# Performance work log

Measured on AMD Instinct MI355X. Metric: run time of the kernel, lower is better.

## Reference

```python
import jax, jax.numpy as jnp
import numpy as np

FACTOR = 0.5  # matches init_kwargs factor


def setup_inputs() -> dict:
    key = jax.random.key(0)
    k1, k2 = jax.random.split(key)
    E, D, N = 1600000, 32, 100000
    edge_data = jax.random.normal(k1, (E, D), dtype=jnp.float32)
    edge_dst = jax.random.randint(k2, (E,), 0, N, dtype=jnp.int64)
    return {"edge_data": edge_data, "edge_dst": edge_dst, "num_nodes": N}


def reference(edge_data, edge_dst, num_nodes):
    # EdgewiseReduce.forward: optional scalar premultiply, then scatter-sum
    # edge features into per-node bins by destination index.
    scaled = edge_data * FACTOR                     # [E, D]
    out = jax.ops.segment_sum(scaled, edge_dst, num_segments=num_nodes)  # [N, D]
    return out
```

## Files before the change

### kernel.cpp

```cpp
#include <hip/hip_runtime.h>
#include <hip/hip_bf16.h>


#define D 32
#define FACTOR 0.5f
#define BSHIFT 7
#define BNODES (1 << BSHIFT)
#define CAPSHIFT 12
#define CAP (1 << CAPSHIFT)

#define S_THREADS 512
#define S_PER_T 2
__global__ __launch_bounds__(S_THREADS)
void scatter_kernel(const int* __restrict__ dst, int* __restrict__ gcursor,
                    int* __restrict__ order, int2* __restrict__ ovf,
                    int* __restrict__ ovf_count, int E, int N, int nb) {
  extern __shared__ int sm[];
  int* lhist = sm;
  int* lcur = sm + nb;
  const int4* dst4 = (const int4*)dst;
  const int n4 = E >> 2;
  const int base4 = blockIdx.x * (S_THREADS * S_PER_T);
  const int i4a = base4 + threadIdx.x;
  const int i4b = i4a + S_THREADS;
  const bool tail_block = (blockIdx.x == gridDim.x - 1);

  for (int i = threadIdx.x; i < nb; i += S_THREADS) lhist[i] = 0;
  __syncthreads();

  int4 va, vb;
  bool ha = (i4a < n4), hb = (i4b < n4);
  if (ha) {
    va = dst4[i4a];
    if ((unsigned)va.x < (unsigned)N) atomicAdd(&lhist[va.x >> BSHIFT], 1);
    if ((unsigned)va.y < (unsigned)N) atomicAdd(&lhist[va.y >> BSHIFT], 1);
    if ((unsigned)va.z < (unsigned)N) atomicAdd(&lhist[va.z >> BSHIFT], 1);
    if ((unsigned)va.w < (unsigned)N) atomicAdd(&lhist[va.w >> BSHIFT], 1);
  }
  if (hb) {
    vb = dst4[i4b];
    if ((unsigned)vb.x < (unsigned)N) atomicAdd(&lhist[vb.x >> BSHIFT], 1);
    if ((unsigned)vb.y < (unsigned)N) atomicAdd(&lhist[vb.y >> BSHIFT], 1);
    if ((unsigned)vb.z < (unsigned)N) atomicAdd(&lhist[vb.z >> BSHIFT], 1);
    if ((unsigned)vb.w < (unsigned)N) atomicAdd(&lhist[vb.w >> BSHIFT], 1);
  }
  if (tail_block) {
    for (int e = (n4 << 2) + threadIdx.x; e < E; e += S_THREADS) {
      int d = dst[e];
      if ((unsigned)d < (unsigned)N) atomicAdd(&lhist[d >> BSHIFT], 1);
    }
  }
  __syncthreads();

  for (int i = threadIdx.x; i < nb; i += S_THREADS) {
    int c = lhist[i];
    lcur[i] = (i << CAPSHIFT) + (c ? atomicAdd(&gcursor[i], c) : 0);
  }
  __syncthreads();

  #define EMIT(dd, ee)                                                        \
    if ((unsigned)(dd) < (unsigned)N) {                                       \
      int bkt = (dd) >> BSHIFT;                                               \
      int pos = atomicAdd(&lcur[bkt], 1);                                     \
      if (pos < ((bkt + 1) << CAPSHIFT)) {                                    \
        order[pos] = ((ee) << BSHIFT) | ((dd) & (BNODES - 1));                \
      } else {                                                                \
        int op = atomicAdd(ovf_count, 1);                                     \
        ovf[op] = make_int2((ee), (dd));                                      \
      }                                                                       \
    }

  if (ha) {
    int e = i4a << 2;
    EMIT(va.x, e + 0)
    EMIT(va.y, e + 1)
    EMIT(va.z, e + 2)
    EMIT(va.w, e + 3)
  }
  if (hb) {
    int e = i4b << 2;
    EMIT(vb.x, e + 0)
    EMIT(vb.y, e + 1)
    EMIT(vb.z, e + 2)
    EMIT(vb.w, e + 3)
  }
  if (tail_block) {
    for (int e = (n4 << 2) + threadIdx.x; e < E; e += S_THREADS) {
      int d = dst[e];
      EMIT(d, e)
    }
  }
  #undef EMIT
}

#define K4_THREADS 512
__global__ __launch_bounds__(K4_THREADS)
void gather_kernel(const float4* __restrict__ data, const int* __restrict__ order,
                   const int* __restrict__ cursor, float4* __restrict__ out,
                   int N) {
  __shared__ int ids[CAP];
  __shared__ int sorted[CAP];
  __shared__ int hist[BNODES];
  __shared__ int offs[BNODES];
  __shared__ int cur[BNODES];

  const int b = blockIdx.x;
  const int base = b << CAPSHIFT;
  int cnt = cursor[b];
  if (cnt > CAP) cnt = CAP;
  if (cnt < 0) cnt = 0;
  const int lo = b << BSHIFT;
  const int tid = threadIdx.x;
  const int grp = tid >> 2;
  const int ln = tid & 3;

  for (int i = tid; i < BNODES; i += K4_THREADS) hist[i] = 0;
  __syncthreads();
  for (int i = tid; i < cnt; i += K4_THREADS) {
    int v = order[base + i];
    ids[i] = v;
    atomicAdd(&hist[v & (BNODES - 1)], 1);
  }
  __syncthreads();

  if (tid < 64) {
    int c0 = hist[2 * tid], c1 = hist[2 * tid + 1];
    int s = c0 + c1;
    int sc = s;
    #pragma unroll
    for (int off = 1; off < 64; off <<= 1) {
      int t = __shfl_up(sc, off);
      if (tid >= off) sc += t;
    }
    int bs = sc - s;
    offs[2 * tid] = bs + c0;
    offs[2 * tid + 1] = bs + c0 + c1;
    cur[2 * tid] = bs;
    cur[2 * tid + 1] = bs + c0;
  }
  __syncthreads();

  for (int i = tid; i < cnt; i += K4_THREADS) {
    int v = ids[i];
    sorted[atomicAdd(&cur[v & (BNODES - 1)], 1)] = v;
  }
  __syncthreads();

  float4 acc0 = make_float4(0.f, 0.f, 0.f, 0.f);
  float4 acc1 = make_float4(0.f, 0.f, 0.f, 0.f);
  int e_ = offs[grp];
  int i = e_ - hist[grp];
  for (; i + 3 < e_; i += 4) {
    int r0 = sorted[i] >> BSHIFT;
    int r1 = sorted[i + 1] >> BSHIFT;
    int r2 = sorted[i + 2] >> BSHIFT;
    int r3 = sorted[i + 3] >> BSHIFT;
    const float4* p0 = data + (size_t)r0 * 8 + ln * 2;
    const float4* p1 = data + (size_t)r1 * 8 + ln * 2;
    const float4* p2 = data + (size_t)r2 * 8 + ln * 2;
    const float4* p3 = data + (size_t)r3 * 8 + ln * 2;
    float4 x0 = p0[0], y0 = p0[1];
    float4 x1 = p1[0], y1 = p1[1];
    float4 x2 = p2[0], y2 = p2[1];
    float4 x3 = p3[0], y3 = p3[1];
    acc0.x += x0.x + x1.x + x2.x + x3.x;
    acc0.y += x0.y + x1.y + x2.y + x3.y;
    acc0.z += x0.z + x1.z + x2.z + x3.z;
    acc0.w += x0.w + x1.w + x2.w + x3.w;
    acc1.x += y0.x + y1.x + y2.x + y3.x;
    acc1.y += y0.y + y1.y + y2.y + y3.y;
    acc1.z += y0.z + y1.z + y2.z + y3.z;
    acc1.w += y0.w + y1.w + y2.w + y3.w;
  }
  for (; i < e_; ++i) {
    int r0 = sorted[i] >> BSHIFT;
    const float4* p0 = data + (size_t)r0 * 8 + ln * 2;
    float4 x0 = p0[0], y0 = p0[1];
    acc0.x += x0.x; acc0.y += x0.y; acc0.z += x0.z; acc0.w += x0.w;
    acc1.x += y0.x; acc1.y += y0.y; acc1.z += y0.z; acc1.w += y0.w;
  }

  int node = lo + grp;
  if (node < N) {
    float4 o0, o1;
    o0.x = acc0.x * FACTOR; o0.y = acc0.y * FACTOR;
    o0.z = acc0.z * FACTOR; o0.w = acc0.w * FACTOR;
    o1.x = acc1.x * FACTOR; o1.y = acc1.y * FACTOR;
    o1.z = acc1.z * FACTOR; o1.w = acc1.w * FACTOR;
    out[(size_t)node * 8 + ln * 2] = o0;
    out[(size_t)node * 8 + ln * 2 + 1] = o1;
  }
}

__global__ void overflow_kernel(const float4* __restrict__ data,
                                const int2* __restrict__ ovf,
                                const int* __restrict__ ovf_count,
                                float* __restrict__ out) {
  int cnt = *ovf_count;
  for (int i = blockIdx.x * blockDim.x + threadIdx.x; i < cnt * 8;
       i += gridDim.x * blockDim.x) {
    int k = i >> 3, q = i & 7;
    int2 ed = ovf[k];
    float4 v = data[(size_t)ed.x * 8 + q];
    float* p = out + (size_t)ed.y * D + q * 4;
    unsafeAtomicAdd(p + 0, v.x * FACTOR);
    unsafeAtomicAdd(p + 1, v.y * FACTOR);
    unsafeAtomicAdd(p + 2, v.z * FACTOR);
    unsafeAtomicAdd(p + 3, v.w * FACTOR);
  }
}

__global__ void atomic_kernel(const float4* __restrict__ edge_data,
                              const int* __restrict__ edge_dst,
                              float* __restrict__ out, int E, int N) {
  int tid = blockIdx.x * blockDim.x + threadIdx.x;
  int e = tid >> 3;
  int q = tid & 7;
  if (e >= E) return;
  int dst = edge_dst[e];
  if (dst < 0 || dst >= N) return;
  float4 v = edge_data[(size_t)e * 8 + q];
  float* p = out + (size_t)dst * D + q * 4;
  unsafeAtomicAdd(p + 0, v.x * FACTOR);
  unsafeAtomicAdd(p + 1, v.y * FACTOR);
  unsafeAtomicAdd(p + 2, v.z * FACTOR);
  unsafeAtomicAdd(p + 3, v.w * FACTOR);
}

extern "C" void kernel_launch(void* const* d_in, const int* in_sizes, int n_in,
                              void* d_out, int out_size, void* d_ws, size_t ws_size,
                              hipStream_t stream) {
  const float4* edge_data = (const float4*)d_in[0];
  const int* edge_dst = (const int*)d_in[1];

  int E = in_sizes[1];
  int N = out_size / D;

  int nb = (N + BNODES - 1) >> BSHIFT;
  size_t ofs_order = 4 + (size_t)nb;
  ofs_order = (ofs_order + 1) & ~(size_t)1;
  size_t ofs_ovf = ofs_order + (size_t)nb * CAP;
  ofs_ovf = (ofs_ovf + 1) & ~(size_t)1;
  size_t need = (ofs_ovf + (size_t)2 * E) * sizeof(int);
  bool pack_ok = ((long long)E << BSHIFT) < (1ll << 31) &&
                 (((long long)nb << CAPSHIFT) < (1ll << 31));

  if (ws_size < need || !pack_ok) {
    float* out = (float*)d_out;
    hipMemsetAsync(d_out, 0, (size_t)out_size * sizeof(float), stream);
    int total = E * 8;
    atomic_kernel<<<(total + 255) / 256, 256, 0, stream>>>(edge_data, edge_dst, out, E, N);
    return;
  }

  int* ws = (int*)d_ws;
  int* ovf_count = ws;
  int* cursor = ws + 4;
  int* order = ws + ofs_order;
  int2* ovf = (int2*)(ws + ofs_ovf);

  hipMemsetAsync(ws, 0, (4 + (size_t)nb) * sizeof(int), stream);

  int epb = S_THREADS * S_PER_T * 4;
  int nblk = (E + epb - 1) / epb;
  if (nblk < 1) nblk = 1;
  size_t lds = (size_t)2 * nb * sizeof(int);
  scatter_kernel<<<nblk, S_THREADS, lds, stream>>>(edge_dst, cursor, order, ovf,
                                                   ovf_count, E, N, nb);

  gather_kernel<<<nb, K4_THREADS, 0, stream>>>(
      edge_data, order, cursor, (float4*)d_out, N);

  overflow_kernel<<<32, 256, 0, stream>>>(edge_data, ovf, ovf_count, (float*)d_out);
}
```

Measured before the change: 328.2 us.

## Stage scatter output in LDS by bucket and use nontemporal gather loads

The scatter kernel now computes a per-block prefix sum over the bucket histogram and stages packed edge entries in shared memory sorted by bucket. It then writes them to the global order array in bucket-contiguous runs, so writes coalesce better than the old scattered per-edge global writes. The gather kernel switches edge-data loads and output stores to nontemporal builtins to reduce cache pollution. In exchange, LDS use grows to about 4*nb ints plus the staging area, which may lower occupancy and adds a fallback path when that exceeds 64KB.

```diff
diff --git a/kernel.cpp b/kernel.cpp
--- a/kernel.cpp
+++ b/kernel.cpp
@@ -9,23 +9,42 @@
 #define CAPSHIFT 12
 #define CAP (1 << CAPSHIFT)
 
+typedef float f32x4 __attribute__((ext_vector_type(4)));
+
+__device__ __forceinline__ float4 ntload(const float4* p) {
+  f32x4 v = __builtin_nontemporal_load((const f32x4*)p);
+  return make_float4(v.x, v.y, v.z, v.w);
+}
+__device__ __forceinline__ void ntstore(float4* p, float4 v) {
+  f32x4 t;
+  t.x = v.x; t.y = v.y; t.z = v.z; t.w = v.w;
+  __builtin_nontemporal_store(t, (f32x4*)p);
+}
+
 #define S_THREADS 512
 #define S_PER_T 2
+#define S_EDGES (S_THREADS * S_PER_T * 4)
 __global__ __launch_bounds__(S_THREADS)
 void scatter_kernel(const int* __restrict__ dst, int* __restrict__ gcursor,
                     int* __restrict__ order, int2* __restrict__ ovf,
                     int* __restrict__ ovf_count, int E, int N, int nb) {
   extern __shared__ int sm[];
   int* lhist = sm;
-  int* lcur = sm + nb;
+  int* lstart = sm + nb;
+  int* lcur = sm + 2 * nb;
+  int* grun = sm + 3 * nb;
+  int* staging = sm + 4 * nb;
+  short* sbkt = (short*)(staging + S_EDGES);
+
   const int4* dst4 = (const int4*)dst;
   const int n4 = E >> 2;
   const int base4 = blockIdx.x * (S_THREADS * S_PER_T);
   const int i4a = base4 + threadIdx.x;
   const int i4b = i4a + S_THREADS;
   const bool tail_block = (blockIdx.x == gridDim.x - 1);
-
-  for (int i = threadIdx.x; i < nb; i += S_THREADS) lhist[i] = 0;
+  const int tid = threadIdx.x;
+
+  for (int i = tid; i < nb; i += S_THREADS) { lhist[i] = 0; lcur[i] = 0; }
   __syncthreads();
 
   int4 va, vb;
@@ -45,52 +64,82 @@
     if ((unsigned)vb.w < (unsigned)N) atomicAdd(&lhist[vb.w >> BSHIFT], 1);
   }
   if (tail_block) {
-    for (int e = (n4 << 2) + threadIdx.x; e < E; e += S_THREADS) {
+    for (int e = (n4 << 2) + tid; e < E; e += S_THREADS) {
       int d = dst[e];
       if ((unsigned)d < (unsigned)N) atomicAdd(&lhist[d >> BSHIFT], 1);
     }
   }
   __syncthreads();
 
-  for (int i = threadIdx.x; i < nb; i += S_THREADS) {
+  for (int i = tid; i < nb; i += S_THREADS) {
     int c = lhist[i];
-    lcur[i] = (i << CAPSHIFT) + (c ? atomicAdd(&gcursor[i], c) : 0);
-  }
-  __syncthreads();
-
-  #define EMIT(dd, ee)                                                        \
+    grun[i] = c ? atomicAdd(&gcursor[i], c) : 0;
+  }
+  if (tid < 64) {
+    int carry = 0;
+    int nchunk = (nb + 63) >> 6;
+    for (int c = 0; c < nchunk; ++c) {
+      int idx = (c << 6) + tid;
+      int v = (idx < nb) ? lhist[idx] : 0;
+      int sc = v;
+      #pragma unroll
+      for (int off = 1; off < 64; off <<= 1) {
+        int t = __shfl_up(sc, off);
+        if (tid >= off) sc += t;
+      }
+      if (idx < nb) lstart[idx] = carry + sc - v;
+      carry += __shfl(sc, 63);
+    }
+  }
+  __syncthreads();
+
+  #define STAGE(dd, ee)                                                       \
     if ((unsigned)(dd) < (unsigned)N) {                                       \
       int bkt = (dd) >> BSHIFT;                                               \
-      int pos = atomicAdd(&lcur[bkt], 1);                                     \
-      if (pos < ((bkt + 1) << CAPSHIFT)) {                                    \
-        order[pos] = ((ee) << BSHIFT) | ((dd) & (BNODES - 1));                \
-      } else {                                                                \
-        int op = atomicAdd(ovf_count, 1);                                     \
-        ovf[op] = make_int2((ee), (dd));                                      \
+      int rank = atomicAdd(&lcur[bkt], 1);                                    \
+      int s = lstart[bkt] + rank;                                             \
+      if (s < S_EDGES) {                                                      \
+        staging[s] = ((ee) << BSHIFT) | ((dd) & (BNODES - 1));                \
+        sbkt[s] = (short)bkt;                                                 \
       }                                                                       \
     }
 
   if (ha) {
     int e = i4a << 2;
-    EMIT(va.x, e + 0)
-    EMIT(va.y, e + 1)
-    EMIT(va.z, e + 2)
-    EMIT(va.w, e + 3)
+    STAGE(va.x, e + 0)
+    STAGE(va.y, e + 1)
+    STAGE(va.z, e + 2)
+    STAGE(va.w, e + 3)
   }
   if (hb) {
     int e = i4b << 2;
-    EMIT(vb.x, e + 0)
-    EMIT(vb.y, e + 1)
-    EMIT(vb.z, e + 2)
-    EMIT(vb.w, e + 3)
+    STAGE(vb.x, e + 0)
+    STAGE(vb.y, e + 1)
+    STAGE(vb.z, e + 2)
+    STAGE(vb.w, e + 3)
   }
   if (tail_block) {
-    for (int e = (n4 << 2) + threadIdx.x; e < E; e += S_THREADS) {
+    for (int e = (n4 << 2) + tid; e < E; e += S_THREADS) {
       int d = dst[e];
-      EMIT(d, e)
-    }
-  }
-  #undef EMIT
+      STAGE(d, e)
+    }
+  }
+  #undef STAGE
+  __syncthreads();
+
+  int tot = lstart[nb - 1] + lhist[nb - 1];
+  if (tot > S_EDGES) tot = S_EDGES;
+  for (int s = tid; s < tot; s += S_THREADS) {
+    int v = staging[s];
+    int bkt = sbkt[s];
+    int grel = grun[bkt] + (s - lstart[bkt]);
+    if (grel < CAP) {
+      order[((size_t)bkt << CAPSHIFT) + grel] = v;
+    } else {
+      int op = atomicAdd(ovf_count, 1);
+      ovf[op] = make_int2(v >> BSHIFT, (bkt << BSHIFT) | (v & (BNODES - 1)));
+    }
+  }
 }
 
 #define K4_THREADS 512
@@ -159,10 +208,10 @@
     const float4* p1 = data + (size_t)r1 * 8 + ln * 2;
     const float4* p2 = data + (size_t)r2 * 8 + ln * 2;
     const float4* p3 = data + (size_t)r3 * 8 + ln * 2;
-    float4 x0 = p0[0], y0 = p0[1];
-    float4 x1 = p1[0], y1 = p1[1];
-    float4 x2 = p2[0], y2 = p2[1];
-    float4 x3 = p3[0], y3 = p3[1];
+    float4 x0 = ntload(p0), y0 = ntload(p0 + 1);
+    float4 x1 = ntload(p1), y1 = ntload(p1 + 1);
+    float4 x2 = ntload(p2), y2 = ntload(p2 + 1);
+    float4 x3 = ntload(p3), y3 = ntload(p3 + 1);
     acc0.x += x0.x + x1.x + x2.x + x3.x;
     acc0.y += x0.y + x1.y + x2.y + x3.y;
     acc0.z += x0.z + x1.z + x2.z + x3.z;
@@ -175,7 +224,7 @@
   for (; i < e_; ++i) {
     int r0 = sorted[i] >> BSHIFT;
     const float4* p0 = data + (size_t)r0 * 8 + ln * 2;
-    float4 x0 = p0[0], y0 = p0[1];
+    float4 x0 = ntload(p0), y0 = ntload(p0 + 1);
     acc0.x += x0.x; acc0.y += x0.y; acc0.z += x0.z; acc0.w += x0.w;
     acc1.x += y0.x; acc1.y += y0.y; acc1.z += y0.z; acc1.w += y0.w;
   }
@@ -187,8 +236,8 @@
     o0.z = acc0.z * FACTOR; o0.w = acc0.w * FACTOR;
     o1.x = acc1.x * FACTOR; o1.y = acc1.y * FACTOR;
     o1.z = acc1.z * FACTOR; o1.w = acc1.w * FACTOR;
-    out[(size_t)node * 8 + ln * 2] = o0;
-    out[(size_t)node * 8 + ln * 2 + 1] = o1;
+    ntstore(out + (size_t)node * 8 + ln * 2, o0);
+    ntstore(out + (size_t)node * 8 + ln * 2 + 1, o1);
   }
 }
 
@@ -244,10 +293,13 @@
   size_t need = (ofs_ovf + (size_t)2 * E) * sizeof(int);
   bool pack_ok = ((long long)E << BSHIFT) < (1ll << 31) &&
                  (((long long)nb << CAPSHIFT) < (1ll << 31));
-
-  if (ws_size < need || !pack_ok) {
+  size_t s_lds = (size_t)4 * nb * sizeof(int) + S_EDGES * sizeof(int) +
+                 S_EDGES * sizeof(short);
+  bool lds_ok = s_lds <= 64 * 1024 && nb > 0;
+
+  if (ws_size < need || !pack_ok || !lds_ok) {
     float* out = (float*)d_out;
-    hipMemsetAsync(d_out, 0, (size_t)out_size * sizeof(float), stream);
+    (void)hipMemsetAsync(d_out, 0, (size_t)out_size * sizeof(float), stream);
     int total = E * 8;
     atomic_kernel<<<(total + 255) / 256, 256, 0, stream>>>(edge_data, edge_dst, out, E, N);
     return;
@@ -259,14 +311,12 @@
   int* order = ws + ofs_order;
   int2* ovf = (int2*)(ws + ofs_ovf);
 
-  hipMemsetAsync(ws, 0, (4 + (size_t)nb) * sizeof(int), stream);
-
-  int epb = S_THREADS * S_PER_T * 4;
-  int nblk = (E + epb - 1) / epb;
+  (void)hipMemsetAsync(ws, 0, (4 + (size_t)nb) * sizeof(int), stream);
+
+  int nblk = (E + S_EDGES - 1) / S_EDGES;
   if (nblk < 1) nblk = 1;
-  size_t lds = (size_t)2 * nb * sizeof(int);
-  scatter_kernel<<<nblk, S_THREADS, lds, stream>>>(edge_dst, cursor, order, ovf,
-                                                   ovf_count, E, N, nb);
+  scatter_kernel<<<nblk, S_THREADS, s_lds, stream>>>(edge_dst, cursor, order, ovf,
+                                                     ovf_count, E, N, nb);
 
   gather_kernel<<<nb, K4_THREADS, 0, stream>>>(
       edge_data, order, cursor, (float4*)d_out, N);
```

Result: faster. 316.4 us (-3.6%).
